# Kernel tuning notes

Measured on AMD Instinct MI355X. Metric: run time of the kernel, lower is better.

## Reference

```python
import jax, jax.numpy as jnp
import numpy as np
from jax import lax

B, T, D = 2, 512, 64   # batch, temporal length, input_dim
H = 64                 # hidden_dims
OUT = 64               # output_dim
REL = 2 * D            # relation_dim = input_dim * 2 (until=True: max & min interval pooling)


def _interval_pool(f, op):
    """f: [B,T,D] -> r: [B,T,T,D] with r[:, i, j] = op-reduction of f[:, i..j] for i <= j.
    Entries with i > j are filled with f[:, i] (degenerate interval); they are never
    read because the downstream backward pooling only reduces over j >= i."""
    Tn = f.shape[1]
    idx = jnp.arange(Tn)

    def step(col, j):
        # col[:, i] holds reduce(f[:, i..j-1]) for i <= j-1, and f[:, i] otherwise
        new = op(col, f[:, j][:, None, :])                      # extend interval to j
        new = jnp.where((idx <= j)[None, :, None], new, f)      # reset i > j rows
        return new, new

    _, cols = lax.scan(step, f, jnp.arange(Tn))  # [T(j), B, T(i), D]
    return jnp.transpose(cols, (1, 2, 0, 3))     # [B, T(i), T(j), D]


def _backward_max_pool(s):
    """s: [B,T,T,C] -> out[:, i] = max_{j >= i} s[:, i, j]  (the 'broadcast' backward pool)."""
    Tn = s.shape[1]
    mask = jnp.arange(Tn)[:, None] <= jnp.arange(Tn)[None, :]   # i <= j
    neg = jnp.asarray(-1e9, s.dtype)
    return jnp.max(jnp.where(mask[None, :, :, None], s, neg), axis=2)


def setup_inputs() -> dict:
    key = jax.random.key(0)
    ks = jax.random.split(key, 7)
    f = jax.random.normal(ks[0], (B, T, D), dtype=jnp.float32)
    # step_linears per __init__: current_dim starts at REL, then hidden_dims
    dims = [(REL + REL, H), (H + REL, H), (H + REL, OUT)]
    params = {}
    for i, (din, dout) in enumerate(dims):
        params[f"W{i}"] = jax.random.normal(ks[1 + 2 * i], (din, dout), jnp.float32) / np.sqrt(din)
        params[f"b{i}"] = jnp.zeros((dout,), jnp.float32)
    return {"f": f, **params}


def reference(f, W0, b0, W1, b1, W2, b2):
    Tn = f.shape[1]
    # until=True: concat max- and min-interval pooling -> [B,T,T,2D]
    r = jnp.concatenate([_interval_pool(f, jnp.maximum),
                         _interval_pool(f, jnp.minimum)], axis=-1)
    current = r[:, :, Tn - 1]  # [B, T, REL] : reductions over suffix intervals [i, T-1]
    for W, b in ((W0, b0), (W1, b1), (W2, b2)):
        # jactorch.add_dim(current, 1, t): broadcast current (indexed by j) over new i axis
        bcast = jnp.broadcast_to(current[:, None, :, :],
                                 (f.shape[0], Tn, Tn, current.shape[-1]))
        li = jnp.concatenate([bcast, r], axis=-1)                 # [B,T,T,C+REL]
        h = jax.nn.sigmoid(jnp.einsum('bijc,co->bijo', li, W) + b)  # MLPLogic, no hidden layers
        current = _backward_max_pool(h)                           # [B,T,out]
    return current
```

## Files before the change

### kernel.cpp

```cpp
#include <hip/hip_runtime.h>
#include <hip/hip_bf16.h>
#include <math.h>

#define B_ 2
#define T_ 512
#define D_ 64

typedef __attribute__((ext_vector_type(8))) short bf16x8;
typedef __attribute__((ext_vector_type(8))) unsigned short u16x8;
typedef __attribute__((ext_vector_type(4))) float f32x4;

static __device__ __forceinline__ unsigned short f2bf(float v) {
    __hip_bfloat16 h = __float2bfloat16(v);
    return *reinterpret_cast<unsigned short*>(&h);
}
static __device__ __forceinline__ float bf2f(unsigned short u) {
    return __uint_as_float(((unsigned)u) << 16);
}
static __device__ __forceinline__ unsigned short maxbits(unsigned short a, unsigned short b) {
    float m = fmaxf(bf2f(a), bf2f(b));
    return (unsigned short)(__float_as_uint(m) >> 16);
}
static __device__ __forceinline__ unsigned short minbits(unsigned short a, unsigned short b) {
    float m = fminf(bf2f(a), bf2f(b));
    return (unsigned short)(__float_as_uint(m) >> 16);
}

__global__ __launch_bounds__(512) void prep_kernel(
    const float* __restrict__ f,
    const float* __restrict__ W0, const float* __restrict__ W1, const float* __restrict__ W2,
    unsigned short* __restrict__ tmax, unsigned short* __restrict__ tmin,
    unsigned short* __restrict__ wf,
    unsigned short* __restrict__ intra,
    float* __restrict__ z0, float* __restrict__ z1, float* __restrict__ z2) {

    __shared__ unsigned short lmax[512][16];
    __shared__ unsigned short lmin[512][16];

    const int blk = blockIdx.x;
    const int tid = threadIdx.x;

    if (blk < 8) {
        const int b = blk & 1;
        const int c0 = (blk >> 1) * 16;
        const int t = tid;

        u16x8 mx[2], mn[2];
#pragma unroll
        for (int h = 0; h < 2; ++h) {
            const float* fp = &f[((size_t)(b * T_ + t) << 6) + c0 + h * 8];
#pragma unroll
            for (int e = 0; e < 8; ++e) {
                unsigned short u = f2bf(fp[e]);
                mx[h][e] = u; mn[h][e] = u;
            }
            size_t base = ((size_t)(b * T_ + t) << 6) + c0 + h * 8;
            *reinterpret_cast<u16x8*>(&tmax[base]) = mx[h];
            *reinterpret_cast<u16x8*>(&tmin[base]) = mn[h];
        }
        for (int k = 1; k <= 9; ++k) {
            *reinterpret_cast<u16x8*>(&lmax[t][0]) = mx[0];
            *reinterpret_cast<u16x8*>(&lmax[t][8]) = mx[1];
            *reinterpret_cast<u16x8*>(&lmin[t][0]) = mn[0];
            *reinterpret_cast<u16x8*>(&lmin[t][8]) = mn[1];
            __syncthreads();
            int t2 = t + (1 << (k - 1));
            if (t2 > T_ - 1) t2 = T_ - 1;
            u16x8 qx0 = *reinterpret_cast<const u16x8*>(&lmax[t2][0]);
            u16x8 qx1 = *reinterpret_cast<const u16x8*>(&lmax[t2][8]);
            u16x8 qn0 = *reinterpret_cast<const u16x8*>(&lmin[t2][0]);
            u16x8 qn1 = *reinterpret_cast<const u16x8*>(&lmin[t2][8]);
#pragma unroll
            for (int e = 0; e < 8; ++e) {
                mx[0][e] = maxbits(mx[0][e], qx0[e]);
                mx[1][e] = maxbits(mx[1][e], qx1[e]);
                mn[0][e] = minbits(mn[0][e], qn0[e]);
                mn[1][e] = minbits(mn[1][e], qn1[e]);
            }
            size_t base = ((size_t)((k * B_ + b) * T_ + t) << 6) + c0;
            *reinterpret_cast<u16x8*>(&tmax[base]) = mx[0];
            *reinterpret_cast<u16x8*>(&tmax[base + 8]) = mx[1];
            *reinterpret_cast<u16x8*>(&tmin[base]) = mn[0];
            *reinterpret_cast<u16x8*>(&tmin[base + 8]) = mn[1];
            __syncthreads();
        }
    } else if (blk < 11) {
        const int layer = blk - 8;
        const float* W = (layer == 0) ? W0 : ((layer == 1) ? W1 : W2);
        const int Coff = (layer == 0) ? 128 : 64;
        const int l = tid & 63;
#pragma unroll
        for (int q = 0; q < 2; ++q) {
            int fr = (tid >> 6) + q * 8;
            int kt = fr >> 2, nt = fr & 3;
#pragma unroll
            for (int e = 0; e < 8; ++e) {
                int row = Coff + kt * 32 + ((l >> 4) << 3) + e;
                int col = nt * 16 + (l & 15);
                wf[((size_t)(layer * 16 + fr) * 64 + l) * 8 + e] = f2bf(W[row * 64 + col]);
            }
        }
    } else if (blk < 43) {
        const int x = blk - 11;
        const int jt = x & 15, b = x >> 4;
        const int jj = tid >> 4, c8 = tid & 15;
        const bool ismin = c8 >= 8;
        unsigned short (*sc)[128] = reinterpret_cast<unsigned short (*)[128]>(lmax);

        const float* fp = &f[((size_t)(b * T_ + jt * 32 + jj) << 6) + (c8 & 7) * 8];
        u16x8 r;
#pragma unroll
        for (int e = 0; e < 8; ++e) r[e] = f2bf(fp[e]);

#pragma unroll
        for (int off = 1; off < 32; off <<= 1) {
            *reinterpret_cast<u16x8*>(&sc[jj][c8 * 8]) = r;
            __syncthreads();
            if (jj >= off) {
                u16x8 q = *reinterpret_cast<const u16x8*>(&sc[jj - off][c8 * 8]);
#pragma unroll
                for (int e = 0; e < 8; ++e)
                    r[e] = ismin ? minbits(r[e], q[e]) : maxbits(r[e], q[e]);
            }
            __syncthreads();
        }
        *reinterpret_cast<u16x8*>(&intra[((size_t)((b * 16 + jt) * 32 + jj) << 7) + c8 * 8]) = r;
    } else {
        int fi = (blk - 43) * 512 + tid;
        float4 z = {0.f, 0.f, 0.f, 0.f};
        if (fi < 16384)       reinterpret_cast<float4*>(z0)[fi] = z;
        else if (fi < 32768)  reinterpret_cast<float4*>(z1)[fi - 16384] = z;
        else                  reinterpret_cast<float4*>(z2)[fi - 32768] = z;
    }
}

__global__ __launch_bounds__(256) void g0_kernel(
    const unsigned short* __restrict__ tabmax,
    const unsigned short* __restrict__ tabmin,
    const float* __restrict__ W0, const float* __restrict__ bias,
    float* __restrict__ g) {

    __shared__ float cur_lds[4][128];

    const int tid = threadIdx.x;
    const int bt0 = blockIdx.x * 4;

    if (tid < 64) {
        int isel = tid >> 4, c8 = tid & 15;
        int bt = bt0 + isel;
        int b = bt >> 9, t = bt & 511;
        int len = T_ - t;
        int kk = 31 - __clz(len);
        int t2 = T_ - (1 << kk);
        const unsigned short* tab = (c8 < 8) ? tabmax : tabmin;
        int cc = (c8 & 7) * 8;
        u16x8 va = *reinterpret_cast<const u16x8*>(&tab[(((size_t)(kk * B_ + b) * T_ + t) << 6) + cc]);
        u16x8 vb = *reinterpret_cast<const u16x8*>(&tab[(((size_t)(kk * B_ + b) * T_ + t2) << 6) + cc]);
#pragma unroll
        for (int e = 0; e < 8; ++e) {
            unsigned short r = (c8 < 8) ? maxbits(va[e], vb[e]) : minbits(va[e], vb[e]);
            cur_lds[isel][c8 * 8 + e] = bf2f(r);
        }
    }
    __syncthreads();

    const int r = tid >> 6, o = tid & 63;
    float s = bias[o];
#pragma unroll 8
    for (int c = 0; c < 128; ++c)
        s = fmaf(cur_lds[r][c], W0[c * 64 + o], s);
    g[((size_t)(bt0 + r) << 6) + o] = s;
}

__global__ __launch_bounds__(256) void g64_kernel(
    const float* __restrict__ cur, const float* __restrict__ W,
    const float* __restrict__ bias, float* __restrict__ g) {
    const int bt = blockIdx.x * 4 + (threadIdx.x >> 6);
    const int o = threadIdx.x & 63;
    float s = bias[o];
    const float* cp = &cur[(size_t)bt << 6];
#pragma unroll 8
    for (int c = 0; c < 64; ++c)
        s = fmaf(cp[c], W[c * 64 + o], s);
    g[((size_t)bt << 6) + o] = s;
}

__global__ __launch_bounds__(512) void pair_kernel(
    const unsigned short* __restrict__ tabmax,
    const unsigned short* __restrict__ tabmin,
    const unsigned short* __restrict__ intra,
    const unsigned short* __restrict__ wf,
    const float* __restrict__ g,
    float* __restrict__ out) {

    int m = blockIdx.x;
    int b, jt, it;
    bool diag;
    if (m < 128) {
        diag = true;
        b = m & 1;
        int idx = m >> 1;
        jt = idx >> 2;
        it = 4 * jt + (idx & 3);
    } else {
        diag = false;
        int m2 = m - 128;
        b = m2 & 1;
        int m3 = m2 >> 1;
        jt = 1;
        while (m3 >= 2 * jt * (jt + 1)) ++jt;
        it = m3 - 2 * jt * (jt - 1);
    }
    const int i0 = it * 8, j0 = jt * 32;

    const int tid = threadIdx.x;
    const int l = tid & 63, w = tid >> 6;
    const int lg = l >> 4, li = l & 15;
    const int pi = i0 + w;

    __shared__ unsigned short intr[32][136];
    __shared__ unsigned short pref[8][136];
    __shared__ unsigned short wlds[16 * 64 * 8];
    __shared__ float gl[32][68];

#pragma unroll
    for (int q = 0; q < 2; ++q) {
        int idx = q * 512 + tid;
        u16x8 v = *reinterpret_cast<const u16x8*>(&wf[(size_t)idx * 8]);
        *reinterpret_cast<u16x8*>(&wlds[idx * 8]) = v;
    }

    {
        int jj = tid >> 4, c4 = tid & 15;
        float4 v = *reinterpret_cast<const float4*>(&g[((size_t)(b * T_ + j0 + jj) << 6) + c4 * 4]);
        *reinterpret_cast<float4*>(&gl[jj][c4 * 4]) = v;
    }

    if (!diag) {
        {
            int jj = tid >> 4, c8 = tid & 15;
            u16x8 v = *reinterpret_cast<const u16x8*>(
                &intra[((size_t)((b * 16 + jt) * 32 + jj) << 7) + c8 * 8]);
            *reinterpret_cast<u16x8*>(&intr[jj][c8 * 8]) = v;
        }
        if (tid < 128) {
            int isel = tid >> 4, c8 = tid & 15;
            int i = i0 + isel;
            int len = j0 - i;
            int kk = 31 - __clz(len);
            int t2 = j0 - (1 << kk);
            const unsigned short* tab = (c8 < 8) ? tabmax : tabmin;
            int cc = (c8 & 7) * 8;
            u16x8 va = *reinterpret_cast<const u16x8*>(&tab[(((size_t)(kk * B_ + b) * T_ + i) << 6) + cc]);
            u16x8 vb = *reinterpret_cast<const u16x8*>(&tab[(((size_t)(kk * B_ + b) * T_ + t2) << 6) + cc]);
            u16x8 r;
#pragma unroll
            for (int e = 0; e < 8; ++e)
                r[e] = (c8 < 8) ? maxbits(va[e], vb[e]) : minbits(va[e], vb[e]);
            *reinterpret_cast<u16x8*>(&pref[isel][c8 * 8]) = r;
        }
    }
    __syncthreads();

    int kk_q[2], t2_q[2];
    if (diag) {
#pragma unroll
        for (int s = 0; s < 2; ++s) {
            int pj = j0 + 16 * s + li;
            int je = (pj < pi) ? pi : pj;
            int len = je - pi + 1;
            kk_q[s] = 31 - __clz(len);
            t2_q[s] = je + 1 - (1 << kk_q[s]);
        }
    }

    f32x4 acc[2][4];
#pragma unroll
    for (int s = 0; s < 2; ++s)
#pragma unroll
        for (int nt = 0; nt < 4; ++nt) acc[s][nt] = (f32x4){0.f, 0.f, 0.f, 0.f};

#pragma unroll
    for (int krt = 0; krt < 4; ++krt) {
        bf16x8 wfr[4];
#pragma unroll
        for (int nt = 0; nt < 4; ++nt)
            wfr[nt] = *reinterpret_cast<const bf16x8*>(&wlds[((krt * 4 + nt) * 64 + l) * 8]);

#pragma unroll
        for (int s = 0; s < 2; ++s) {
            const int pjj = 16 * s + li;
            bf16x8 av;
            if (!diag) {
                u16x8 iv = *reinterpret_cast<const u16x8*>(&intr[pjj][(krt * 4 + lg) * 8]);
                u16x8 pv = *reinterpret_cast<const u16x8*>(&pref[w][(krt * 4 + lg) * 8]);
                if (krt < 2) {
#pragma unroll
                    for (int e = 0; e < 8; ++e) av[e] = (short)maxbits(iv[e], pv[e]);
                } else {
#pragma unroll
                    for (int e = 0; e < 8; ++e) av[e] = (short)minbits(iv[e], pv[e]);
                }
            } else {
                const int c8 = krt * 4 + lg;
                const unsigned short* tab = (krt < 2) ? tabmax : tabmin;
                const int cc = (c8 & 7) * 8;
                const int kku = kk_q[s], t2u = t2_q[s];
                u16x8 va = *reinterpret_cast<const u16x8*>(&tab[(((size_t)(kku * B_ + b) * T_ + pi) << 6) + cc]);
                u16x8 vb = *reinterpret_cast<const u16x8*>(&tab[(((size_t)(kku * B_ + b) * T_ + t2u) << 6) + cc]);
                if (krt < 2) {
#pragma unroll
                    for (int e = 0; e < 8; ++e) av[e] = (short)maxbits(va[e], vb[e]);
                } else {
#pragma unroll
                    for (int e = 0; e < 8; ++e) av[e] = (short)minbits(va[e], vb[e]);
                }
            }
#pragma unroll
            for (int nt = 0; nt < 4; ++nt)
                acc[s][nt] = __builtin_amdgcn_mfma_f32_16x16x32_bf16(av, wfr[nt], acc[s][nt], 0, 0, 0);
        }
    }

#pragma unroll
    for (int nt = 0; nt < 4; ++nt) {
        const int o = nt * 16 + li;
        float vm = -1e9f;
#pragma unroll
        for (int s = 0; s < 2; ++s)
#pragma unroll
            for (int r = 0; r < 4; ++r) {
                int jj = 16 * s + lg * 4 + r;
                float v = acc[s][nt][r] + gl[jj][o];
                if (!diag || (j0 + jj >= pi)) vm = fmaxf(vm, v);
            }
        vm = fmaxf(vm, __shfl_xor(vm, 16));
        vm = fmaxf(vm, __shfl_xor(vm, 32));
        if (l < 16) {
            float h = 1.0f / (1.0f + __expf(-vm));
            atomicMax((int*)out + (((size_t)(b * T_ + pi) << 6) + o), __float_as_int(h));
        }
    }
}

extern "C" void kernel_launch(void* const* d_in, const int* in_sizes, int n_in,
                              void* d_out, int out_size, void* d_ws, size_t ws_size,
                              hipStream_t stream) {
    const float* f  = (const float*)d_in[0];
    const float* W0 = (const float*)d_in[1];
    const float* b0 = (const float*)d_in[2];
    const float* W1 = (const float*)d_in[3];
    const float* b1 = (const float*)d_in[4];
    const float* W2 = (const float*)d_in[5];
    const float* b2 = (const float*)d_in[6];
    float* outp = (float*)d_out;

    unsigned short* tabmax = (unsigned short*)d_ws;
    unsigned short* tabmin = tabmax + 10 * B_ * T_ * 64;
    unsigned short* wf     = tabmin + 10 * B_ * T_ * 64;
    unsigned short* intra  = wf + 3 * 16 * 64 * 8;
    float* cur1 = (float*)(intra + B_ * 16 * 32 * 128);
    float* cur2 = cur1 + B_ * T_ * 64;
    float* gbuf = cur2 + B_ * T_ * 64;

    prep_kernel<<<dim3(139), dim3(512), 0, stream>>>(f, W0, W1, W2,
                                                     tabmax, tabmin, wf, intra,
                                                     cur1, cur2, outp);

    const dim3 pgrid(B_ * 544);
    const dim3 ggrid(B_ * T_ / 4);

    g0_kernel<<<ggrid, dim3(256), 0, stream>>>(tabmax, tabmin, W0, b0, gbuf);
    pair_kernel<<<pgrid, dim3(512), 0, stream>>>(tabmax, tabmin, intra,
                                                 wf + 0 * 8192, gbuf, cur1);

    g64_kernel<<<ggrid, dim3(256), 0, stream>>>(cur1, W1, b1, gbuf);
    pair_kernel<<<pgrid, dim3(512), 0, stream>>>(tabmax, tabmin, intra,
                                                 wf + 1 * 8192, gbuf, cur2);

    g64_kernel<<<ggrid, dim3(256), 0, stream>>>(cur2, W2, b2, gbuf);
    pair_kernel<<<pgrid, dim3(512), 0, stream>>>(tabmax, tabmin, intra,
                                                 wf + 2 * 8192, gbuf, outp);
}
```

Measured before the change: 77.59 us.

## Replace atomicMax output with per-tile partial buffer and reduce in follow-up kernel

The pair kernel no longer applies sigmoid and atomicMax into the output. It writes raw pre-sigmoid maxima into a partial buffer indexed by j-tile, and a new reduction kernel takes the max over tiles, applies sigmoid and computes the next layer's projection. A final kernel produces the output. This removes atomic contention and the zero-init blocks in prep, at the cost of an extra launch plus partial-buffer traffic.

```diff
diff --git a/kernel.cpp b/kernel.cpp
--- a/kernel.cpp
+++ b/kernel.cpp
@@ -31,8 +31,7 @@
     const float* __restrict__ W0, const float* __restrict__ W1, const float* __restrict__ W2,
     unsigned short* __restrict__ tmax, unsigned short* __restrict__ tmin,
     unsigned short* __restrict__ wf,
-    unsigned short* __restrict__ intra,
-    float* __restrict__ z0, float* __restrict__ z1, float* __restrict__ z2) {
+    unsigned short* __restrict__ intra) {
 
     __shared__ unsigned short lmax[512][16];
     __shared__ unsigned short lmin[512][16];
@@ -100,7 +99,7 @@
                 wf[((size_t)(layer * 16 + fr) * 64 + l) * 8 + e] = f2bf(W[row * 64 + col]);
             }
         }
-    } else if (blk < 43) {
+    } else {
         const int x = blk - 11;
         const int jt = x & 15, b = x >> 4;
         const int jj = tid >> 4, c8 = tid & 15;
@@ -125,12 +124,6 @@
             __syncthreads();
         }
         *reinterpret_cast<u16x8*>(&intra[((size_t)((b * 16 + jt) * 32 + jj) << 7) + c8 * 8]) = r;
-    } else {
-        int fi = (blk - 43) * 512 + tid;
-        float4 z = {0.f, 0.f, 0.f, 0.f};
-        if (fi < 16384)       reinterpret_cast<float4*>(z0)[fi] = z;
-        else if (fi < 32768)  reinterpret_cast<float4*>(z1)[fi - 16384] = z;
-        else                  reinterpret_cast<float4*>(z2)[fi - 32768] = z;
     }
 }
 
@@ -172,17 +165,41 @@
     g[((size_t)(bt0 + r) << 6) + o] = s;
 }
 
-__global__ __launch_bounds__(256) void g64_kernel(
-    const float* __restrict__ cur, const float* __restrict__ W,
-    const float* __restrict__ bias, float* __restrict__ g) {
+__global__ __launch_bounds__(256) void gred_kernel(
+    const float* __restrict__ partial,
+    const float* __restrict__ W, const float* __restrict__ bias,
+    float* __restrict__ g) {
+
+    __shared__ float hl[4][64];
+
+    const int tid = threadIdx.x;
+    const int bt0 = blockIdx.x * 4;
+    const int r = tid >> 6, o = tid & 63;
+    const int bt = bt0 + r;
+    const int t = bt & 511;
+
+    float m = -1e9f;
+    for (int jt = t >> 5; jt < 16; ++jt)
+        m = fmaxf(m, partial[((size_t)jt * (B_ * T_) + bt) * 64 + o]);
+    hl[r][o] = 1.0f / (1.0f + __expf(-m));
+    __syncthreads();
+
+    float s = bias[o];
+#pragma unroll 8
+    for (int c = 0; c < 64; ++c)
+        s = fmaf(hl[r][c], W[c * 64 + o], s);
+    g[((size_t)bt << 6) + o] = s;
+}
+
+__global__ __launch_bounds__(256) void fin_kernel(
+    const float* __restrict__ partial, float* __restrict__ out) {
     const int bt = blockIdx.x * 4 + (threadIdx.x >> 6);
     const int o = threadIdx.x & 63;
-    float s = bias[o];
-    const float* cp = &cur[(size_t)bt << 6];
-#pragma unroll 8
-    for (int c = 0; c < 64; ++c)
-        s = fmaf(cp[c], W[c * 64 + o], s);
-    g[((size_t)bt << 6) + o] = s;
+    const int t = bt & 511;
+    float m = -1e9f;
+    for (int jt = t >> 5; jt < 16; ++jt)
+        m = fmaxf(m, partial[((size_t)jt * (B_ * T_) + bt) * 64 + o]);
+    out[((size_t)bt << 6) + o] = 1.0f / (1.0f + __expf(-m));
 }
 
 __global__ __launch_bounds__(512) void pair_kernel(
@@ -191,7 +208,7 @@
     const unsigned short* __restrict__ intra,
     const unsigned short* __restrict__ wf,
     const float* __restrict__ g,
-    float* __restrict__ out) {
+    float* __restrict__ partial) {
 
     int m = blockIdx.x;
     int b, jt, it;
@@ -336,10 +353,8 @@
             }
         vm = fmaxf(vm, __shfl_xor(vm, 16));
         vm = fmaxf(vm, __shfl_xor(vm, 32));
-        if (l < 16) {
-            float h = 1.0f / (1.0f + __expf(-vm));
-            atomicMax((int*)out + (((size_t)(b * T_ + pi) << 6) + o), __float_as_int(h));
-        }
+        if (l < 16)
+            partial[((size_t)jt * (B_ * T_) + b * T_ + pi) * 64 + o] = vm;
     }
 }
 
@@ -359,26 +374,26 @@
     unsigned short* tabmin = tabmax + 10 * B_ * T_ * 64;
     unsigned short* wf     = tabmin + 10 * B_ * T_ * 64;
     unsigned short* intra  = wf + 3 * 16 * 64 * 8;
-    float* cur1 = (float*)(intra + B_ * 16 * 32 * 128);
-    float* cur2 = cur1 + B_ * T_ * 64;
-    float* gbuf = cur2 + B_ * T_ * 64;
-
-    prep_kernel<<<dim3(139), dim3(512), 0, stream>>>(f, W0, W1, W2,
-                                                     tabmax, tabmin, wf, intra,
-                                                     cur1, cur2, outp);
+    float* gbuf    = (float*)(intra + B_ * 16 * 32 * 128);
+    float* partial = gbuf + B_ * T_ * 64;
+
+    prep_kernel<<<dim3(43), dim3(512), 0, stream>>>(f, W0, W1, W2,
+                                                    tabmax, tabmin, wf, intra);
 
     const dim3 pgrid(B_ * 544);
     const dim3 ggrid(B_ * T_ / 4);
 
     g0_kernel<<<ggrid, dim3(256), 0, stream>>>(tabmax, tabmin, W0, b0, gbuf);
     pair_kernel<<<pgrid, dim3(512), 0, stream>>>(tabmax, tabmin, intra,
-                                                 wf + 0 * 8192, gbuf, cur1);
-
-    g64_kernel<<<ggrid, dim3(256), 0, stream>>>(cur1, W1, b1, gbuf);
+                                                 wf + 0 * 8192, gbuf, partial);
+
+    gred_kernel<<<ggrid, dim3(256), 0, stream>>>(partial, W1, b1, gbuf);
     pair_kernel<<<pgrid, dim3(512), 0, stream>>>(tabmax, tabmin, intra,
-                                                 wf + 1 * 8192, gbuf, cur2);
-
-    g64_kernel<<<ggrid, dim3(256), 0, stream>>>(cur2, W2, b2, gbuf);
+                                                 wf + 1 * 8192, gbuf, partial);
+
+    gred_kernel<<<ggrid, dim3(256), 0, stream>>>(partial, W2, b2, gbuf);
     pair_kernel<<<pgrid, dim3(512), 0, stream>>>(tabmax, tabmin, intra,
-                                                 wf + 2 * 8192, gbuf, outp);
-}
+                                                 wf + 2 * 8192, gbuf, partial);
+
+    fin_kernel<<<ggrid, dim3(256), 0, stream>>>(partial, outp);
+}
```

Measured after the change: 84.56 us. 9.0% more time.
